# Optimization experiments

Hardware: AMD Instinct MI355X
Metric: run time of the kernel (lower is better)

The kernel has to match this reference:

```python
import jax, jax.numpy as jnp
import numpy as np

B, N, E, P, PH, H = 4, 512, 768, 64, 32, 8
D = E // H  # 96
FFN = 3072

def _ln(x, g, b, eps=1e-5):
    mu = jnp.mean(x, axis=-1, keepdims=True)
    var = jnp.mean((x - mu) ** 2, axis=-1, keepdims=True)
    return (x - mu) * jax.lax.rsqrt(var + eps) * g + b

def setup_inputs() -> dict:
    key = jax.random.key(0)
    ks = iter(jax.random.split(key, 80))
    def f(*s):
        return jax.random.normal(next(ks), s, jnp.float32) * 0.02
    ones = lambda *s: jnp.ones(s, jnp.float32)
    zeros = lambda *s: jnp.zeros(s, jnp.float32)
    return {
        'x': jax.random.normal(next(ks), (B, N, E), jnp.float32),
        'pair': jax.random.normal(next(ks), (B, N, N, P), jnp.float32) * 0.5,
        'attn_mask': zeros(B, 1, N, N),
        'op_mask': ones(B, N, 1),
        'op_norm': ones(1) / N,
        'nlist': jax.random.randint(next(ks), (B, N, 64), 0, N),
        'wq': f(E, E), 'wk': f(E, E), 'wv': f(E, E),
        'wg': f(E, E), 'bg': zeros(E),
        'wo': f(E, E), 'bo': zeros(E),
        'ln_pair_g': ones(P), 'ln_pair_b': zeros(P),
        'wb': f(H, P), 'bb': zeros(H),
        'ln_attn_g': ones(E), 'ln_attn_b': zeros(E),
        'ln_ffn_g': ones(E), 'ln_ffn_b': zeros(E),
        'w_ffn1': f(FFN, E), 'b_ffn1': zeros(FFN),
        'w_ffn2': f(E, FFN), 'b_ffn2': zeros(E),
        'ln_opm_g': ones(E), 'ln_opm_b': zeros(E),
        'w_opm_in': f(2 * PH, E), 'b_opm_in': zeros(2 * PH),
        'w_opm_out': f(P, PH * PH), 'b_opm_out': zeros(P),
        'ln_tm_g': ones(P), 'ln_tm_b': zeros(P),
        'w_tm_abp': f(2 * PH, P), 'b_tm_abp': zeros(2 * PH),
        'w_tm_abg': f(2 * PH, P), 'b_tm_abg': zeros(2 * PH),
        'w_tm_g': f(P, P), 'b_tm_g': zeros(P),
        'w_tm_z': f(P, PH), 'b_tm_z': zeros(P),
        'ln_tmo_g': ones(PH), 'ln_tmo_b': zeros(PH),
        'ln_pffn_g': ones(P), 'ln_pffn_b': zeros(P),
        'w_pffn1': f(P, P), 'b_pffn1': zeros(P),
        'w_pffn2': f(P, P), 'b_pffn2': zeros(P),
    }

def _forward(x, pair, attn_mask, op_mask, op_norm, wq, wk, wv, wg, bg, wo, bo,
             ln_pair_g, ln_pair_b, wb, bb, ln_attn_g, ln_attn_b,
             ln_ffn_g, ln_ffn_b, w_ffn1, b_ffn1, w_ffn2, b_ffn2,
             ln_opm_g, ln_opm_b, w_opm_in, b_opm_in, w_opm_out, b_opm_out,
             ln_tm_g, ln_tm_b, w_tm_abp, b_tm_abp, w_tm_abg, b_tm_abg,
             w_tm_g, b_tm_g, w_tm_z, b_tm_z, ln_tmo_g, ln_tmo_b,
             ln_pffn_g, ln_pffn_b, w_pffn1, b_pffn1, w_pffn2, b_pffn2):
    Bx, Nx, _ = x.shape
    # --- gated pair-bias self-attention (pre-LN, eval mode: dropout = identity) ---
    h = _ln(x, ln_attn_g, ln_attn_b)
    pn = _ln(pair, ln_pair_g, ln_pair_b)               # AtomAttention pair LayerNorm
    bias = jnp.einsum('bijp,hp->bhij', pn, wb) + bb[None, :, None, None]
    q = (h @ wq.T).reshape(Bx, Nx, H, D).transpose(0, 2, 1, 3) * (D ** -0.5)
    k = (h @ wk.T).reshape(Bx, Nx, H, D).transpose(0, 2, 1, 3)
    v = (h @ wv.T).reshape(Bx, Nx, H, D).transpose(0, 2, 1, 3)
    attn = jax.nn.softmax(jnp.einsum('bhid,bhjd->bhij', q, k) + attn_mask + bias, axis=-1)
    o = jnp.einsum('bhij,bhjd->bhid', attn, v).transpose(0, 2, 1, 3).reshape(Bx, Nx, E)
    o = jax.nn.sigmoid(h @ wg.T + bg) * o              # sigmoid output gate
    x = x + (o @ wo.T + bo)
    # --- atom transition MLP ---
    h = _ln(x, ln_ffn_g, ln_ffn_b)
    x = x + (jax.nn.gelu(h @ w_ffn1.T + b_ffn1, approximate=False) @ w_ffn2.T + b_ffn2)
    # --- OuterProduct pair update (fused: avoids [B,N,N,PH*PH] intermediate) ---
    h = _ln(x, ln_opm_g, ln_opm_b)
    ab = (h @ w_opm_in.T + b_opm_in) * op_mask
    a_o, b_o = jnp.split(ab, 2, axis=-1)               # each [B,N,PH]
    z = jnp.einsum('bid,bje,pde->bijp', a_o, b_o, w_opm_out.reshape(P, PH, PH)) + b_opm_out
    pair = pair + z * op_norm
    # --- triangle multiplication ---
    zp = _ln(pair, ln_tm_g, ln_tm_b)
    gpr = zp @ w_tm_g.T + b_tm_g                       # gate (no sigmoid, matches source)
    ab = (zp @ w_tm_abp.T + b_tm_abp) * jax.nn.sigmoid(zp @ w_tm_abg.T + b_tm_abg)
    a_t, b_t = jnp.split(ab, 2, axis=-1)               # each [B,N,N,PH]
    t = jnp.einsum('bijh,bkjh->bhik', a_t, b_t) + jnp.einsum('bjih,bjkh->bhik', a_t, b_t)
    t = _ln(t.transpose(0, 2, 3, 1), ln_tmo_g, ln_tmo_b) @ w_tm_z.T + b_tm_z
    pair = pair + gpr * t
    # --- pair transition MLP ---
    zp = _ln(pair, ln_pffn_g, ln_pffn_b)
    pair = pair + (jax.nn.gelu(zp @ w_pffn1.T + b_pffn1, approximate=False) @ w_pffn2.T + b_pffn2)
    return x, pair

def reference(x, pair, attn_mask, op_mask, op_norm, nlist, wq, wk, wv, wg, bg, wo, bo,
              ln_pair_g, ln_pair_b, wb, bb, ln_attn_g, ln_attn_b,
              ln_ffn_g, ln_ffn_b, w_ffn1, b_ffn1, w_ffn2, b_ffn2,
              ln_opm_g, ln_opm_b, w_opm_in, b_opm_in, w_opm_out, b_opm_out,
              ln_tm_g, ln_tm_b, w_tm_abp, b_tm_abp, w_tm_abg, b_tm_abg,
              w_tm_g, b_tm_g, w_tm_z, b_tm_z, ln_tmo_g, ln_tmo_b,
              ln_pffn_g, ln_pffn_b, w_pffn1, b_pffn1, w_pffn2, b_pffn2):
    del nlist  # accepted by the torch module but unused in the math
    return _forward(x, pair, attn_mask, op_mask, op_norm, wq, wk, wv, wg, bg, wo, bo,
                    ln_pair_g, ln_pair_b, wb, bb, ln_attn_g, ln_attn_b,
                    ln_ffn_g, ln_ffn_b, w_ffn1, b_ffn1, w_ffn2, b_ffn2,
                    ln_opm_g, ln_opm_b, w_opm_in, b_opm_in, w_opm_out, b_opm_out,
                    ln_tm_g, ln_tm_b, w_tm_abp, b_tm_abp, w_tm_abg, b_tm_abg,
                    w_tm_g, b_tm_g, w_tm_z, b_tm_z, ln_tmo_g, ln_tmo_b,
                    ln_pffn_g, ln_pffn_b, w_pffn1, b_pffn1, w_pffn2, b_pffn2)
```

## Files before the change

### kernel.cpp

```cpp
#include <hip/hip_runtime.h>
#include <hip/hip_bf16.h>
#include <math.h>

#define Nn 512
#define Ee 768
#define Pp 64
#define PHh 32
#define Hh 8
#define Dd 96
#define NNe 262144
#define LNEPS 1e-5f

typedef __attribute__((ext_vector_type(8))) short bf8;
typedef __attribute__((ext_vector_type(4))) short bf4;
typedef __attribute__((ext_vector_type(4))) float f32x4;
#define MFMA(a,b,c) __builtin_amdgcn_mfma_f32_16x16x32_bf16(a,b,c,0,0,0)

__device__ __forceinline__ short f2bf(float f) {
  unsigned u = __builtin_bit_cast(unsigned, f);
  unsigned r = (u + 0x7fffu + ((u >> 16) & 1u)) >> 16;
  return (short)r;
}
__device__ __forceinline__ float bf2f(short s) {
  unsigned u = ((unsigned)(unsigned short)s) << 16;
  return __builtin_bit_cast(float, u);
}

__device__ __forceinline__ float wave_red_sum(float v) {
#pragma unroll
  for (int off = 32; off > 0; off >>= 1) v += __shfl_xor(v, off);
  return v;
}
__device__ __forceinline__ float gelu_exact(float v) {
  return 0.5f * v * (1.f + erff(v * 0.70710678118654752f));
}
__device__ __forceinline__ float sigmoidf_(float v) {
  return 1.f / (1.f + expf(-v));
}

__global__ __launch_bounds__(256) void castw_kernel(
    const float* __restrict__ wq, const float* __restrict__ wk,
    const float* __restrict__ wv, const float* __restrict__ wg,
    const float* __restrict__ wo, const float* __restrict__ f1,
    const float* __restrict__ f2, const float* __restrict__ wop,
    short* __restrict__ dst, float qs) {
  long i = (long)blockIdx.x * 256 + threadIdx.x;
  float v;
  if (i < 589824) v = wq[i] * qs;
  else if (i < 1179648) v = wk[i - 589824];
  else if (i < 1769472) v = wv[i - 1179648];
  else if (i < 2359296) v = wg[i - 1769472];
  else if (i < 2949120) v = wo[i - 2359296];
  else if (i < 5308416) v = f1[i - 2949120];
  else if (i < 7667712) v = f2[i - 5308416];
  else if (i < 7716864) v = wop[i - 7667712];
  else return;
  dst[i] = f2bf(v);
}

__global__ __launch_bounds__(256) void castw2_kernel(
    const float* __restrict__ wb, const float* __restrict__ abp,
    const float* __restrict__ abg, const float* __restrict__ wtg,
    const float* __restrict__ wtz, const float* __restrict__ p1,
    const float* __restrict__ p2, short* __restrict__ dst) {
  int i = blockIdx.x * 256 + threadIdx.x;
  float v;
  if (i < 512) v = wb[i];
  else if (i < 4608) v = abp[i - 512];
  else if (i < 8704) v = abg[i - 4608];
  else if (i < 12800) v = wtg[i - 8704];
  else if (i < 14848) v = wtz[i - 12800];
  else if (i < 18944) v = p1[i - 14848];
  else if (i < 23040) v = p2[i - 18944];
  else return;
  dst[i] = f2bf(v);
}

__global__ __launch_bounds__(256) void ln_bf_kernel(const float* __restrict__ in,
                                                    short* __restrict__ out,
                                                    const float* __restrict__ gam,
                                                    const float* __restrict__ bet, int C) {
  int row = blockIdx.x;
  const float* xr = in + (long)row * C;
  short* yr = out + (long)row * C;
  float s = 0.f, ss = 0.f;
  for (int c = threadIdx.x; c < C; c += 256) { float v = xr[c]; s += v; ss += v * v; }
  s = wave_red_sum(s); ss = wave_red_sum(ss);
  __shared__ float sm[4][2];
  int wv = threadIdx.x >> 6, lane = threadIdx.x & 63;
  if (lane == 0) { sm[wv][0] = s; sm[wv][1] = ss; }
  __syncthreads();
  float ts = sm[0][0] + sm[1][0] + sm[2][0] + sm[3][0];
  float tss = sm[0][1] + sm[1][1] + sm[2][1] + sm[3][1];
  float mu = ts / C;
  float var = tss / C - mu * mu;
  float rs = rsqrtf(var + LNEPS);
  for (int c = threadIdx.x; c < C; c += 256) {
    float v = xr[c];
    yr[c] = f2bf((v - mu) * rs * gam[c] + bet[c]);
  }
}

__global__ __launch_bounds__(256) void gemm_bf(
    const short* __restrict__ A, int lda, long asB, long asH,
    const short* __restrict__ Bm, int ldb, long bsB, long bsH,
    float* __restrict__ outF, int ldf, long fsB, long fsH,
    short* __restrict__ outB, int ldob,
    const float* __restrict__ resid, int ldr, long rsB, long rsH,
    const float* __restrict__ bias,
    int M, int N, int K, int act, int vtrans, int Hdim) {
  int bz = blockIdx.z, bb = bz / Hdim, hh = bz % Hdim;
  A += bb * asB + hh * asH;
  Bm += bb * bsB + hh * bsH;
  if (outF) outF += bb * fsB + hh * fsH;
  if (outB) outB += bb * fsB + hh * fsH;
  if (resid) resid += bb * rsB + hh * rsH;
  __shared__ __align__(16) short As[64 * 72];
  __shared__ __align__(16) short Bs[64 * 72];
  int m0 = blockIdx.y * 64, n0 = blockIdx.x * 64;
  int tid = threadIdx.x;
  int wv = tid >> 6, lane = tid & 63;
  int wr = wv >> 1, wc = wv & 1;
  int lhi = lane >> 4, llo = lane & 15;
  int r4 = tid >> 2, c8 = (tid & 3) * 8;
  f32x4 acc[2][2] = {};
  for (int k0 = 0; k0 < K; k0 += 64) {
// ... 122 lines not shown
      }
    }
  }
}

__global__ __launch_bounds__(256) void gemm_ffn1(
    const short* __restrict__ A, const short* __restrict__ W,
    short* __restrict__ outB, const float* __restrict__ bias) {
  __shared__ __align__(16) short As[128 * 40];
  __shared__ __align__(16) short Bs[128 * 40];
  int m0 = blockIdx.y * 128, n0 = blockIdx.x * 128;
  int tid = threadIdx.x;
  int wv = tid >> 6, lane = tid & 63;
  int wr = wv >> 1, wc = wv & 1;
  int lhi = lane >> 4, llo = lane & 15;
  int r4 = tid >> 2, c8 = (tid & 3) * 8;
  f32x4 acc[4][4] = {};
  for (int k0 = 0; k0 < 768; k0 += 32) {
    *(bf8*)&As[r4 * 40 + c8] = *(const bf8*)(A + (long)(m0 + r4) * 768 + k0 + c8);
    *(bf8*)&As[(r4 + 64) * 40 + c8] =
        *(const bf8*)(A + (long)(m0 + r4 + 64) * 768 + k0 + c8);
    *(bf8*)&Bs[r4 * 40 + c8] = *(const bf8*)(W + (long)(n0 + r4) * 768 + k0 + c8);
    *(bf8*)&Bs[(r4 + 64) * 40 + c8] =
        *(const bf8*)(W + (long)(n0 + r4 + 64) * 768 + k0 + c8);
    __syncthreads();
    bf8 af[4], bfm[4];
#pragma unroll
    for (int mi = 0; mi < 4; ++mi)
      af[mi] = *(const bf8*)&As[(wr * 64 + mi * 16 + llo) * 40 + lhi * 8];
#pragma unroll
    for (int ni = 0; ni < 4; ++ni)
      bfm[ni] = *(const bf8*)&Bs[(wc * 64 + ni * 16 + llo) * 40 + lhi * 8];
#pragma unroll
    for (int mi = 0; mi < 4; ++mi)
#pragma unroll
      for (int ni = 0; ni < 4; ++ni)
        acc[mi][ni] = MFMA(af[mi], bfm[ni], acc[mi][ni]);
    __syncthreads();
  }
#pragma unroll
  for (int mi = 0; mi < 4; ++mi) {
    int gmb = m0 + wr * 64 + mi * 16 + lhi * 4;
#pragma unroll
    for (int ni = 0; ni < 4; ++ni) {
      int gn = n0 + wc * 64 + ni * 16 + llo;
      float bv = bias[gn];
#pragma unroll
      for (int r = 0; r < 4; ++r)
        outB[(long)(gmb + r) * 3072 + gn] = f2bf(gelu_exact(acc[mi][ni][r] + bv));
    }
  }
}

__global__ __launch_bounds__(256) void attn_fused(
    const short* __restrict__ q_bf, const short* __restrict__ k_bf,
    const short* __restrict__ bias_bf, const float* __restrict__ mask,
    short* __restrict__ out_bf) {
  int it = blockIdx.x, h = blockIdx.y, b = blockIdx.z;
  int tid = threadIdx.x;
  int wv = tid >> 6, lane = tid & 63;
  int lhi = lane >> 4, llo = lane & 15;
  int i0 = it * 16;
  long qoff = ((long)(b * 512 + i0)) * 768 + h * 96;
  bf8 qf[3];
#pragma unroll
  for (int ks = 0; ks < 3; ++ks)
    qf[ks] = *(const bf8*)(q_bf + qoff + (long)llo * 768 + ks * 32 + lhi * 8);
  long koff = ((long)b * 512) * 768 + h * 96;
  long bioff = (long)(b * 8 + h) * NNe + (long)i0 * 512;
  long moff = (long)b * NNe + (long)i0 * 512;
  float sv[8][4];
  int jb0 = wv * 128;
#pragma unroll
  for (int jf = 0; jf < 8; ++jf) {
    int jb = jb0 + jf * 16;
    f32x4 acc = {0.f, 0.f, 0.f, 0.f};
#pragma unroll
    for (int ks = 0; ks < 3; ++ks) {
      bf8 kf = *(const bf8*)(k_bf + koff + (long)(jb + llo) * 768 + ks * 32 + lhi * 8);
      acc = MFMA(qf[ks], kf, acc);
    }
#pragma unroll
    for (int r = 0; r < 4; ++r) {
      int irow = lhi * 4 + r;
      int j = jb + llo;
      float bia = bf2f(bias_bf[bioff + (long)irow * 512 + j]);
      float mk = mask[moff + (long)irow * 512 + j];
      sv[jf][r] = acc[r] + bia + mk;
    }
  }
  __shared__ float redA[4][20];
  __shared__ float redB[4][20];
  float rmax[4];
#pragma unroll
  for (int r = 0; r < 4; ++r) {
    float m = sv[0][r];
#pragma unroll
    for (int jf = 1; jf < 8; ++jf) m = fmaxf(m, sv[jf][r]);
#pragma unroll
    for (int off = 1; off < 16; off <<= 1) m = fmaxf(m, __shfl_xor(m, off, 16));
    if (llo == 0) redA[wv][lhi * 4 + r] = m;
  }
  __syncthreads();
#pragma unroll
  for (int r = 0; r < 4; ++r) {
    int row = lhi * 4 + r;
    rmax[r] = fmaxf(fmaxf(redA[0][row], redA[1][row]),
                    fmaxf(redA[2][row], redA[3][row]));
  }
  float rsum[4] = {0.f, 0.f, 0.f, 0.f};
#pragma unroll
  for (int jf = 0; jf < 8; ++jf)
#pragma unroll
    for (int r = 0; r < 4; ++r) {
      float e = __expf(sv[jf][r] - rmax[r]);
      sv[jf][r] = e;
      rsum[r] += e;
    }
#pragma unroll
  for (int r = 0; r < 4; ++r) {
#pragma unroll
    for (int off = 1; off < 16; off <<= 1) rsum[r] += __shfl_xor(rsum[r], off, 16);
    if (llo == 0) redB[wv][lhi * 4 + r] = rsum[r];
  }
  __syncthreads();
#pragma unroll
  for (int r = 0; r < 4; ++r) {
    int row = lhi * 4 + r;
    float s = redB[0][row] + redB[1][row] + redB[2][row] + redB[3][row];
    float inv = 1.f / s;
#pragma unroll
    for (int jf = 0; jf < 8; ++jf) {
      int j = jb0 + jf * 16 + llo;
      out_bf[bioff + (long)row * 512 + j] = f2bf(sv[jf][r] * inv);
    }
  }
}

__global__ __launch_bounds__(256) void opmask_kernel(float* __restrict__ ab,
                                                     const float* __restrict__ mask,
                                                     short* __restrict__ bo_bf) {
  int idx = blockIdx.x * 256 + threadIdx.x;
  if (idx < 131072) {
    float v = ab[idx] * mask[idx >> 6];
    ab[idx] = v;
    int ch = idx & 63;
    if (ch >= 32) bo_bf[(idx >> 6) * 32 + ch - 32] = f2bf(v);
  }
}

__global__ __launch_bounds__(256) void opm_T_kernel(const float* __restrict__ ab,
                                                    const float* __restrict__ w,
                                                    short* __restrict__ T) {
  int p = blockIdx.y;
  int row = blockIdx.x * 8 + threadIdx.y;
  int e = threadIdx.x;
  const float* a = ab + (long)row * 64;
  const float* wp = w + p * 1024 + e;
  float acc = 0.f;
#pragma unroll
  for (int d = 0; d < 32; ++d) acc += a[d] * wp[d * 32];
  T[((long)row * 64 + p) * 32 + e] = f2bf(acc);
}

__global__ __launch_bounds__(256) void pair_bias_mfma(
    const float* __restrict__ pair, const float* __restrict__ gam,
    const float* __restrict__ bet, const short* __restrict__ wb_a,
    const float* __restrict__ bbv, short* __restrict__ bias) {
  __shared__ __align__(16) short Zb[64 * 72];
  __shared__ __align__(16) short Wb[16 * 72];
  __shared__ float sp[4][2][72];
  int tid = threadIdx.x;
  long e0 = (long)blockIdx.x * 64;
  int b = (int)(e0 >> 18);
  long ein = e0 & (NNe - 1);
  const float* base = pair + e0 * 64;
  for (int l = tid; l < 1024; l += 256) {
    int h = l >> 6, c = l & 63;
    Wb[h * 72 + c] = (h < 8) ? wb_a[h * 64 + c] : (short)0;
  }
  int e = tid & 63, q = tid >> 6;
  f32x4 v4[4];
  float s = 0.f, ss = 0.f;
#pragma unroll
  for (int k = 0; k < 4; ++k) {
    v4[k] = *(const f32x4*)(base + (long)e * 64 + q * 16 + k * 4);
#pragma unroll
    for (int u = 0; u < 4; ++u) { float v = v4[k][u]; s += v; ss += v * v; }
  }
  sp[q][0][e] = s; sp[q][1][e] = ss;
  __syncthreads();
  float ts = sp[0][0][e] + sp[1][0][e] + sp[2][0][e] + sp[3][0][e];
  float tss = sp[0][1][e] + sp[1][1][e] + sp[2][1][e] + sp[3][1][e];
  float mu = ts * 0.015625f, var = tss * 0.015625f - mu * mu;
  float rs = rsqrtf(var + LNEPS);
#pragma unroll
  for (int k = 0; k < 4; ++k) {
    bf4 pk;
#pragma unroll
    for (int u = 0; u < 4; ++u) {
      int c = q * 16 + k * 4 + u;
      pk[u] = f2bf((v4[k][u] - mu) * rs * gam[c] + bet[c]);
    }
    *(bf4*)&Zb[e * 72 + q * 16 + k * 4] = pk;
  }
  __syncthreads();
  int wv = tid >> 6, lane = tid & 63;
  int lhi = lane >> 4, llo = lane & 15;
  int n0 = wv * 16;
  f32x4 acc = {0.f, 0.f, 0.f, 0.f};
#pragma unroll
  for (int ks = 0; ks < 2; ++ks) {
    bf8 a = *(const bf8*)&Wb[llo * 72 + ks * 32 + lhi * 8];
    bf8 bz = *(const bf8*)&Zb[(n0 + llo) * 72 + ks * 32 + lhi * 8];
    acc = MFMA(a, bz, acc);
  }
  int elem = n0 + llo;
#pragma unroll
  for (int r = 0; r < 4; ++r) {
    int h = lhi * 4 + r;
    if (h < 8) bias[(long)(b * 8 + h) * NNe + ein + elem] = f2bf(acc[r] + bbv[h]);
  }
}

__global__ __launch_bounds__(256) void opm_ab_fused(
    const float* __restrict__ pair_in, const short* __restrict__ Tb,
    const short* __restrict__ bo_bf, const float* __restrict__ b_out,
    const float* __restrict__ op_norm, const float* __restrict__ gam,
    const float* __restrict__ bet, const short* __restrict__ wp_a,
    const float* __restrict__ b_abp, const short* __restrict__ wg_a,
    const float* __restrict__ b_abg,
    short* __restrict__ aN, short* __restrict__ bN) {
  int jt = blockIdx.x;
  int i = blockIdx.y;
  int tid = threadIdx.x;
  __shared__ __align__(16) short Tsb[64 * 40];
  __shared__ __align__(16) short Bob[64 * 40];
  __shared__ __align__(16) short Zb[64 * 72];
  __shared__ __align__(16) short Wp[64 * 72];
  __shared__ __align__(16) short Wg[64 * 72];
  __shared__ float spS[64][9];
  __shared__ float spQ[64][9];
  int wv = tid >> 6, lane = tid & 63;
  int wr = wv >> 1, wc = wv & 1;
  int lhi = lane >> 4, llo = lane & 15;
  int chb = wr * 32 + lhi * 4;
  {
    int p = tid >> 2, e8 = (tid & 3) * 8;
    *(bf8*)&Tsb[p * 40 + e8] = *(const bf8*)(Tb + (long)i * 2048 + p * 32 + e8);
    *(bf8*)&Bob[p * 40 + e8] = *(const bf8*)(bo_bf + (long)(jt * 64 + p) * 32 + e8);
  }
  for (int l = tid; l < 512; l += 256) {
    int r = l >> 3, c8 = (l & 7) * 8;
    *(bf8*)&Wp[r * 72 + c8] = *(const bf8*)(wp_a + r * 64 + c8);
    *(bf8*)&Wg[r * 72 + c8] = *(const bf8*)(wg_a + r * 64 + c8);
  }
  long ebase = (long)i * 512 + jt * 64;
  const float* pbase = pair_in + ebase * 64;
  f32x4 x[2][2];
#pragma unroll
  for (int mi = 0; mi < 2; ++mi)
#pragma unroll
    for (int ni = 0; ni < 2; ++ni)
      x[mi][ni] = *(const f32x4*)(pbase + (long)(wc * 32 + ni * 16 + llo) * 64 +
                                  chb + mi * 16);
  __syncthreads();
  f32x4 acc[2][2] = {};
  {
    bf8 a0 = *(const bf8*)&Tsb[(wr * 32 + llo) * 40 + lhi * 8];
    bf8 a1 = *(const bf8*)&Tsb[(wr * 32 + 16 + llo) * 40 + lhi * 8];
    bf8 b0 = *(const bf8*)&Bob[(wc * 32 + llo) * 40 + lhi * 8];
    bf8 b1 = *(const bf8*)&Bob[(wc * 32 + 16 + llo) * 40 + lhi * 8];
    acc[0][0] = MFMA(a0, b0, acc[0][0]);
    acc[0][1] = MFMA(a0, b1, acc[0][1]);
    acc[1][0] = MFMA(a1, b0, acc[1][0]);
    acc[1][1] = MFMA(a1, b1, acc[1][1]);
  }
  float nrm = op_norm[0];
#pragma unroll
  for (int mi = 0; mi < 2; ++mi) {
    f32x4 bo4 = *(const f32x4*)(b_out + chb + mi * 16);
#pragma unroll
    for (int ni = 0; ni < 2; ++ni)
#pragma unroll
      for (int r = 0; r < 4; ++r)
        x[mi][ni][r] += (acc[mi][ni][r] + bo4[r]) * nrm;
  }
#pragma unroll
  for (int ni = 0; ni < 2; ++ni) {
    float s = 0.f, ss = 0.f;
#pragma unroll
    for (int mi = 0; mi < 2; ++mi)
#pragma unroll
      for (int r = 0; r < 4; ++r) { float v = x[mi][ni][r]; s += v; ss += v * v; }
    int e = wc * 32 + ni * 16 + llo;
    spS[e][wr * 4 + lhi] = s;
    spQ[e][wr * 4 + lhi] = ss;
  }
  __syncthreads();
  float mu1[2], rs1[2];
#pragma unroll
  for (int ni = 0; ni < 2; ++ni) {
    int e = wc * 32 + ni * 16 + llo;
    float s = 0.f, q2 = 0.f;
#pragma unroll
    for (int k = 0; k < 8; ++k) { s += spS[e][k]; q2 += spQ[e][k]; }
    float mu = s * 0.015625f, var = q2 * 0.015625f - mu * mu;
    mu1[ni] = mu; rs1[ni] = rsqrtf(var + LNEPS);
  }
#pragma unroll
  for (int mi = 0; mi < 2; ++mi) {
    f32x4 gv = *(const f32x4*)(gam + chb + mi * 16);
    f32x4 bv = *(const f32x4*)(bet + chb + mi * 16);
#pragma unroll
    for (int ni = 0; ni < 2; ++ni) {
      int e = wc * 32 + ni * 16 + llo;
      bf4 pk;
#pragma unroll
      for (int r = 0; r < 4; ++r)
        pk[r] = f2bf((x[mi][ni][r] - mu1[ni]) * rs1[ni] * gv[r] + bv[r]);
      *(bf4*)&Zb[e * 72 + chb + mi * 16] = pk;
    }
  }
  __syncthreads();
  f32x4 ap[2][2] = {};
  f32x4 ag[2][2] = {};
#pragma unroll
  for (int ks = 0; ks < 2; ++ks) {
    bf8 z0 = *(const bf8*)&Zb[(wr * 32 + llo) * 72 + ks * 32 + lhi * 8];
    bf8 z1 = *(const bf8*)&Zb[(wr * 32 + 16 + llo) * 72 + ks * 32 + lhi * 8];
    bf8 p0 = *(const bf8*)&Wp[(wc * 32 + llo) * 72 + ks * 32 + lhi * 8];
    bf8 p1 = *(const bf8*)&Wp[(wc * 32 + 16 + llo) * 72 + ks * 32 + lhi * 8];
    bf8 g0 = *(const bf8*)&Wg[(wc * 32 + llo) * 72 + ks * 32 + lhi * 8];
    bf8 g1 = *(const bf8*)&Wg[(wc * 32 + 16 + llo) * 72 + ks * 32 + lhi * 8];
    ap[0][0] = MFMA(z0, p0, ap[0][0]);
    ap[0][1] = MFMA(z0, p1, ap[0][1]);
    ap[1][0] = MFMA(z1, p0, ap[1][0]);
    ap[1][1] = MFMA(z1, p1, ap[1][1]);
    ag[0][0] = MFMA(z0, g0, ag[0][0]);
    ag[0][1] = MFMA(z0, g1, ag[0][1]);
    ag[1][0] = MFMA(z1, g0, ag[1][0]);
    ag[1][1] = MFMA(z1, g1, ag[1][1]);
  }
#pragma unroll
  for (int mi = 0; mi < 2; ++mi) {
    int elemb = wr * 32 + mi * 16 + lhi * 4;
#pragma unroll
    for (int ni = 0; ni < 2; ++ni) {
      int ch = wc * 32 + ni * 16 + llo;
      float bp = b_abp[ch], bg = b_abg[ch];
      bf4 pack;
#pragma unroll
      for (int r = 0; r < 4; ++r)
        pack[r] = f2bf((ap[mi][ni][r] + bp) * sigmoidf_(ag[mi][ni][r] + bg));
      short* dst = (ch < 32) ? (aN + (long)ch * NNe) : (bN + (long)(ch - 32) * NNe);
      *(bf4*)(dst + ebase + elemb) = pack;
    }
  }
}

__global__ __launch_bounds__(512) void tm_tri_mfma(const short* __restrict__ aN,
                                                   const short* __restrict__ bN,
                                                   short* __restrict__ t_out) {
  int lin = blockIdx.z * 16 + blockIdx.y * 4 + blockIdx.x;
  int vid = (lin & 7) * 64 + (lin >> 3);
  int h = vid >> 4;
  int rem = vid & 15;
  int i0 = (rem >> 2) * 128, k0 = (rem & 3) * 128;
  const short* A = aN + (long)h * NNe;
  const short* B = bN + (long)h * NNe;
  __shared__ __align__(16) short A1[128 * 40];
  __shared__ __align__(16) short B1[128 * 40];
  __shared__ __align__(16) short A2[128 * 40];
  __shared__ __align__(16) short B2[128 * 40];
  int tid = threadIdx.x;
  int wv = tid >> 6, lane = tid & 63;
  int wr = wv >> 2, wc = wv & 3;
  int lhi = lane >> 4, llo = lane & 15;
  int r1 = tid >> 2, cp = (tid & 3) * 8;
  int s2 = tid >> 5, cg = (tid & 31) * 4;
  f32x4 acc[4][2] = {};
  for (int j0 = 0; j0 < 512; j0 += 32) {
    *(bf8*)&A1[r1 * 40 + cp] = *(const bf8*)(A + (long)(i0 + r1) * 512 + j0 + cp);
    *(bf8*)&B1[r1 * 40 + cp] = *(const bf8*)(B + (long)(k0 + r1) * 512 + j0 + cp);
    bf4 va0 = *(const bf4*)(A + (long)(j0 + 2 * s2) * 512 + i0 + cg);
    bf4 va1 = *(const bf4*)(A + (long)(j0 + 2 * s2 + 1) * 512 + i0 + cg);
    bf4 vb0 = *(const bf4*)(B + (long)(j0 + 2 * s2) * 512 + k0 + cg);
    bf4 vb1 = *(const bf4*)(B + (long)(j0 + 2 * s2 + 1) * 512 + k0 + cg);
#pragma unroll
    for (int q = 0; q < 4; ++q) {
      unsigned pa = (unsigned)(unsigned short)va0[q] |
                    ((unsigned)(unsigned short)va1[q] << 16);
      unsigned pb = (unsigned)(unsigned short)vb0[q] |
                    ((unsigned)(unsigned short)vb1[q] << 16);
      *(unsigned*)&A2[(cg + q) * 40 + 2 * s2] = pa;
      *(unsigned*)&B2[(cg + q) * 40 + 2 * s2] = pb;
    }
    __syncthreads();
    bf8 bfr[2], dfr[2];
#pragma unroll
    for (int ni = 0; ni < 2; ++ni) {
      bfr[ni] = *(const bf8*)&B1[(wc * 32 + ni * 16 + llo) * 40 + lhi * 8];
      dfr[ni] = *(const bf8*)&B2[(wc * 32 + ni * 16 + llo) * 40 + lhi * 8];
    }
#pragma unroll
    for (int mi = 0; mi < 4; ++mi) {
      bf8 a = *(const bf8*)&A1[(wr * 64 + mi * 16 + llo) * 40 + lhi * 8];
      acc[mi][0] = MFMA(a, bfr[0], acc[mi][0]);
      acc[mi][1] = MFMA(a, bfr[1], acc[mi][1]);
    }
#pragma unroll
    for (int mi = 0; mi < 4; ++mi) {
      bf8 c = *(const bf8*)&A2[(wr * 64 + mi * 16 + llo) * 40 + lhi * 8];
      acc[mi][0] = MFMA(c, dfr[0], acc[mi][0]);
      acc[mi][1] = MFMA(c, dfr[1], acc[mi][1]);
    }
    __syncthreads();
  }
  short* tp = t_out + (long)h * NNe;
#pragma unroll
  for (int mi = 0; mi < 4; ++mi)
#pragma unroll
    for (int ni = 0; ni < 2; ++ni) {
      int row = i0 + wr * 64 + mi * 16 + lhi * 4;
      int col = k0 + wc * 32 + ni * 16 + llo;
#pragma unroll
      for (int r = 0; r < 4; ++r) tp[(long)(row + r) * 512 + col] = f2bf(acc[mi][ni][r]);
    }
}

__global__ __launch_bounds__(256) void upd_pffn_fused(
    const float* __restrict__ pin, float* __restrict__ pout,
    const short* __restrict__ t_in,
    const short* __restrict__ Tb, const short* __restrict__ bo_bf,
    const float* __restrict__ b_out, const float* __restrict__ op_norm,
    const float* __restrict__ g_tm, const float* __restrict__ b_tm,
    const short* __restrict__ wg_a, const float* __restrict__ b_g,
    const short* __restrict__ wz_a, const float* __restrict__ b_z,
    const float* __restrict__ g_tmo, const float* __restrict__ b_tmo,
    const float* __restrict__ g_pf, const float* __restrict__ b_pf,
    const short* __restrict__ w1_a, const float* __restrict__ b1,
    const short* __restrict__ w2_a, const float* __restrict__ b2) {
  __shared__ __align__(16) short Zb[64 * 72];
  __shared__ __align__(16) short Tlb[64 * 40];
  __shared__ __align__(16) short Wbuf[64 * 72];
  __shared__ __align__(16) short Wzb[64 * 40];
  __shared__ __align__(16) short Tsb[64 * 40];
  __shared__ __align__(16) short Bob[64 * 40];
  __shared__ float spS[64][9];
  __shared__ float spQ[64][9];
  __shared__ float spB[4][2][72];
  int tid = threadIdx.x;
  long e0 = (long)blockIdx.x * 64;
  int i = (int)(e0 >> 9);
  int jt = (int)((e0 >> 6) & 7);
  int wv = tid >> 6, lane = tid & 63;
  int wr = wv >> 1, wc = wv & 1;
  int lhi = lane >> 4, llo = lane & 15;
  int chb = wr * 32 + lhi * 4;
  int r0 = tid >> 3, c0 = (tid & 7) * 8;
  int r1 = (tid + 256) >> 3, c1 = ((tid + 256) & 7) * 8;
  bf8 w1r0, w1r1, w2r0, w2r1;
  {
    *(bf8*)&Wbuf[r0 * 72 + c0] = *(const bf8*)(wg_a + r0 * 64 + c0);
    *(bf8*)&Wbuf[r1 * 72 + c1] = *(const bf8*)(wg_a + r1 * 64 + c1);
    w1r0 = *(const bf8*)(w1_a + r0 * 64 + c0);
    w1r1 = *(const bf8*)(w1_a + r1 * 64 + c1);
    w2r0 = *(const bf8*)(w2_a + r0 * 64 + c0);
    w2r1 = *(const bf8*)(w2_a + r1 * 64 + c1);
    int rz = tid >> 2, cz = (tid & 3) * 8;
    *(bf8*)&Wzb[rz * 40 + cz] = *(const bf8*)(wz_a + rz * 32 + cz);
    int p = tid >> 2, e8 = (tid & 3) * 8;
    *(bf8*)&Tsb[p * 40 + e8] = *(const bf8*)(Tb + (long)i * 2048 + p * 32 + e8);
    *(bf8*)&Bob[p * 40 + e8] = *(const bf8*)(bo_bf + (long)(jt * 64 + p) * 32 + e8);
  }
  f32x4 x[2][2];
#pragma unroll
  for (int mi = 0; mi < 2; ++mi)
#pragma unroll
    for (int ni = 0; ni < 2; ++ni)
      x[mi][ni] = *(const f32x4*)(pin + (e0 + wc * 32 + ni * 16 + llo) * 64 +
                                  chb + mi * 16);
  int te = tid & 63, tq = tid >> 6;
  float tt[8];
  {
    float sB = 0.f, ssB = 0.f;
#pragma unroll
    for (int k = 0; k < 8; ++k) {
      float v = bf2f(t_in[(long)(tq * 8 + k) * NNe + e0 + te]);
      tt[k] = v; sB += v; ssB += v * v;
    }
    spB[tq][0][te] = sB; spB[tq][1][te] = ssB;
  }
  __syncthreads();
  {
    float ts = spB[0][0][te] + spB[1][0][te] + spB[2][0][te] + spB[3][0][te];
    float tss = spB[0][1][te] + spB[1][1][te] + spB[2][1][te] + spB[3][1][te];
    float mu = ts * 0.03125f, var = tss * 0.03125f - mu * mu;
    float rs = rsqrtf(var + LNEPS);
    bf8 pk;
#pragma unroll
    for (int k = 0; k < 8; ++k) {
      int c = tq * 8 + k;
      pk[k] = f2bf((tt[k] - mu) * rs * g_tmo[c] + b_tmo[c]);
    }
    *(bf8*)&Tlb[te * 40 + tq * 8] = pk;
  }
  {
    f32x4 acc[2][2] = {};
    bf8 a0 = *(const bf8*)&Tsb[(wr * 32 + llo) * 40 + lhi * 8];
    bf8 a1 = *(const bf8*)&Tsb[(wr * 32 + 16 + llo) * 40 + lhi * 8];
    bf8 b0 = *(const bf8*)&Bob[(wc * 32 + llo) * 40 + lhi * 8];
    bf8 b1 = *(const bf8*)&Bob[(wc * 32 + 16 + llo) * 40 + lhi * 8];
    acc[0][0] = MFMA(a0, b0, acc[0][0]);
    acc[0][1] = MFMA(a0, b1, acc[0][1]);
    acc[1][0] = MFMA(a1, b0, acc[1][0]);
    acc[1][1] = MFMA(a1, b1, acc[1][1]);
    float nrm = op_norm[0];
#pragma unroll
    for (int mi = 0; mi < 2; ++mi) {
      f32x4 bo4 = *(const f32x4*)(b_out + chb + mi * 16);
#pragma unroll
      for (int ni = 0; ni < 2; ++ni)
#pragma unroll
        for (int r = 0; r < 4; ++r)
          x[mi][ni][r] += (acc[mi][ni][r] + bo4[r]) * nrm;
    }
  }
#pragma unroll
  for (int ni = 0; ni < 2; ++ni) {
    float s = 0.f, ss = 0.f;
#pragma unroll
    for (int mi = 0; mi < 2; ++mi)
#pragma unroll
      for (int r = 0; r < 4; ++r) { float v = x[mi][ni][r]; s += v; ss += v * v; }
    int e = wc * 32 + ni * 16 + llo;
    spS[e][wr * 4 + lhi] = s;
    spQ[e][wr * 4 + lhi] = ss;
  }
  __syncthreads();
  float mu1[2], rs1[2];
#pragma unroll
// ... 172 lines not shown
  const float* w_ffn2 = (const float*)d_in[23];
  const float* b_ffn2 = (const float*)d_in[24];
  const float* ln_opm_g = (const float*)d_in[25];
  const float* ln_opm_b = (const float*)d_in[26];
  const float* w_opm_in = (const float*)d_in[27];
  const float* b_opm_in = (const float*)d_in[28];
  const float* w_opm_out = (const float*)d_in[29];
  const float* b_opm_out = (const float*)d_in[30];
  const float* ln_tm_g = (const float*)d_in[31];
  const float* ln_tm_b = (const float*)d_in[32];
  const float* w_tm_abp = (const float*)d_in[33];
  const float* b_tm_abp = (const float*)d_in[34];
  const float* w_tm_abg = (const float*)d_in[35];
  const float* b_tm_abg = (const float*)d_in[36];
  const float* w_tm_g = (const float*)d_in[37];
  const float* b_tm_g = (const float*)d_in[38];
  const float* w_tm_z = (const float*)d_in[39];
  const float* b_tm_z = (const float*)d_in[40];
  const float* ln_tmo_g = (const float*)d_in[41];
  const float* ln_tmo_b = (const float*)d_in[42];
  const float* ln_pffn_g = (const float*)d_in[43];
  const float* ln_pffn_b = (const float*)d_in[44];
  const float* w_pffn1 = (const float*)d_in[45];
  const float* b_pffn1 = (const float*)d_in[46];
  const float* w_pffn2 = (const float*)d_in[47];
  const float* b_pffn2 = (const float*)d_in[48];

  float* ws = (float*)d_ws;
  short* wbf = (short*)ws;
  short* wq_bf = wbf + 0;
  short* wo_bf = wbf + 2359296;
  short* wf1_bf = wbf + 2949120;
  short* wf2_bf = wbf + 5308416;
  short* wop_bf = wbf + 7667712;
  short* wb_a = wbf + 7716864;
  short* wabp_a = wbf + 7717376;
  short* wabg_a = wbf + 7721472;
  short* wtg_a = wbf + 7725568;
  short* wtz_a = wbf + 7729664;
  short* wp1_a = wbf + 7731712;
  short* wp2_a = wbf + 7735808;

  short* h_bf = (short*)(ws + 3869952);
  short* q_bf = (short*)(ws + 4656384);
  short* k_bf = (short*)(ws + 5442816);
  short* vT_bf = (short*)(ws + 6229248);
  float* gb = ws + 7015680;
  short* gb_bf = (short*)(ws + 10161408);
  float* x1b = ws + 10947840;
  short* biasb_bf = (short*)(ws + 12520704);
  short* attn_bf = (short*)(ws + 16715008);
  short* mffn_bf = (short*)(ws + 20909312);
  float* abb = ws + 24055040;
  short* abb_bf = (short*)(ws + 24186112);
  short* Tb_bf = (short*)(ws + 24218880);
  short* aNb = (short*)(ws + 4656384);
  short* bNb = (short*)(ws + 8850688);
  short* t_bf = (short*)(ws + 13044992);

  float* xo = (float*)d_out;
  float* pair1 = xo + 1572864;

  const float qscale = 0.1020620726159658f;

  castw_kernel<<<30144, 256, 0, stream>>>(wq, wk, wv_, wg, wo, w_ffn1, w_ffn2, w_opm_in,
                                          wbf, qscale);
  castw2_kernel<<<90, 256, 0, stream>>>(wb, w_tm_abp, w_tm_abg, w_tm_g, w_tm_z,
                                        w_pffn1, w_pffn2, wb_a);
  ln_bf_kernel<<<2048, 256, 0, stream>>>(x, h_bf, ln_attn_g, ln_attn_b, 768);
  gemm_qkvg<<<dim3(24, 16, 1), 256, 0, stream>>>(h_bf, wq_bf, q_bf, k_bf, vT_bf, gb, bg);
  pair_bias_mfma<<<16384, 256, 0, stream>>>(pair, ln_pair_g, ln_pair_b, wb_a, bb, biasb_bf);
  attn_fused<<<dim3(32, 8, 4), 256, 0, stream>>>(q_bf, k_bf, biasb_bf, attn_mask, attn_bf);
  gemm_bf<<<dim3(2, 8, 32), 256, 0, stream>>>(attn_bf, 512, 2097152, 262144,
                                              vT_bf, 512, 393216, 49152,
                                              nullptr, 0, 393216, 96, gb_bf, 768,
                                              gb, 768, 393216, 96, nullptr,
                                              512, 96, 512, 2, 0, 8);
  gemm_bf<<<dim3(12, 32, 1), 256, 0, stream>>>(gb_bf, 768, 0, 0, wo_bf, 768, 0, 0,
                                               x1b, 768, 0, 0, nullptr, 0,
                                               x, 768, 0, 0, bo,
                                               2048, 768, 768, 0, 0, 1);
  ln_bf_kernel<<<2048, 256, 0, stream>>>(x1b, h_bf, ln_ffn_g, ln_ffn_b, 768);
  gemm_ffn1<<<dim3(24, 16, 1), 256, 0, stream>>>(h_bf, wf1_bf, mffn_bf, b_ffn1);
  gemm_bf<<<dim3(12, 32, 1), 256, 0, stream>>>(mffn_bf, 3072, 0, 0, wf2_bf, 3072, 0, 0,
                                               xo, 768, 0, 0, nullptr, 0,
                                               x1b, 768, 0, 0, b_ffn2,
                                               2048, 768, 3072, 0, 0, 1);
  ln_bf_kernel<<<2048, 256, 0, stream>>>(xo, h_bf, ln_opm_g, ln_opm_b, 768);
  gemm_bf<<<dim3(1, 32, 1), 256, 0, stream>>>(h_bf, 768, 0, 0, wop_bf, 768, 0, 0,
                                              abb, 64, 0, 0, nullptr, 0,
                                              nullptr, 0, 0, 0, b_opm_in,
                                              2048, 64, 768, 0, 0, 1);
  opmask_kernel<<<512, 256, 0, stream>>>(abb, op_mask, abb_bf);
  opm_T_kernel<<<dim3(256, 64, 1), dim3(32, 8, 1), 0, stream>>>(abb, w_opm_out, Tb_bf);
  for (int b = 0; b < 4; ++b) {
    const float* pin = pair + (long)b * NNe * 64;
    float* pbb = pair1 + (long)b * NNe * 64;
    opm_ab_fused<<<dim3(8, 512, 1), 256, 0, stream>>>(
        pin, Tb_bf + (long)b * 1048576, abb_bf + (long)b * 16384, b_opm_out, op_norm,
        ln_tm_g, ln_tm_b, wabp_a, b_tm_abp, wabg_a, b_tm_abg, aNb, bNb);
    tm_tri_mfma<<<dim3(4, 4, 32), 512, 0, stream>>>(aNb, bNb, t_bf);
    upd_pffn_fused<<<4096, 256, 0, stream>>>(
        pin, pbb, t_bf, Tb_bf + (long)b * 1048576, abb_bf + (long)b * 16384,
        b_opm_out, op_norm,
        ln_tm_g, ln_tm_b, wtg_a, b_tm_g, wtz_a, b_tm_z,
        ln_tmo_g, ln_tmo_b, ln_pffn_g, ln_pffn_b, wp1_a, b_pffn1, wp2_a, b_pffn2);
  }
}
```

Baseline: 907.0 us.

## Batch pair-track kernels across batch, cache bf16 pair copy, merge small kernels

Removes the per-batch loop so opm_ab_fused, tm_tri_mfma and upd_pffn_fused each launch once over all four batches, backed by larger workspace buffers. pair_bias_mfma now also writes a bf16 copy of pair, which later kernels read instead of the fp32 tensor, halving that traffic. The two weight-cast kernels are merged, opmask is folded into opm_T_kernel, and the two N=768 output GEMMs move to a new 128x128-tile kernel. Reading pair as bf16 in the residual path adds precision loss, and the extra bf16 write plus the larger workspace add memory cost.

```diff
diff --git a/kernel.cpp b/kernel.cpp
--- a/kernel.cpp
+++ b/kernel.cpp
@@ -43,6 +43,10 @@
     const float* __restrict__ wv, const float* __restrict__ wg,
     const float* __restrict__ wo, const float* __restrict__ f1,
     const float* __restrict__ f2, const float* __restrict__ wop,
+    const float* __restrict__ wb, const float* __restrict__ abp,
+    const float* __restrict__ abg, const float* __restrict__ wtg,
+    const float* __restrict__ wtz, const float* __restrict__ p1,
+    const float* __restrict__ p2,
     short* __restrict__ dst, float qs) {
   long i = (long)blockIdx.x * 256 + threadIdx.x;
   float v;
@@ -54,24 +58,13 @@
   else if (i < 5308416) v = f1[i - 2949120];
   else if (i < 7667712) v = f2[i - 5308416];
   else if (i < 7716864) v = wop[i - 7667712];
-  else return;
-  dst[i] = f2bf(v);
-}
-
-__global__ __launch_bounds__(256) void castw2_kernel(
-    const float* __restrict__ wb, const float* __restrict__ abp,
-    const float* __restrict__ abg, const float* __restrict__ wtg,
-    const float* __restrict__ wtz, const float* __restrict__ p1,
-    const float* __restrict__ p2, short* __restrict__ dst) {
-  int i = blockIdx.x * 256 + threadIdx.x;
-  float v;
-  if (i < 512) v = wb[i];
-  else if (i < 4608) v = abp[i - 512];
-  else if (i < 8704) v = abg[i - 4608];
-  else if (i < 12800) v = wtg[i - 8704];
-  else if (i < 14848) v = wtz[i - 12800];
-  else if (i < 18944) v = p1[i - 14848];
-  else if (i < 23040) v = p2[i - 18944];
+  else if (i < 7717376) v = wb[i - 7716864];
+  else if (i < 7721472) v = abp[i - 7717376];
+  else if (i < 7725568) v = abg[i - 7721472];
+  else if (i < 7729664) v = wtg[i - 7725568];
+  else if (i < 7731712) v = wtz[i - 7729664];
+  else if (i < 7735808) v = p1[i - 7731712];
+  else if (i < 7739904) v = p2[i - 7735808];
   else return;
   dst[i] = f2bf(v);
 }
@@ -300,6 +293,56 @@
   }
 }
 
+__global__ __launch_bounds__(256) void gemm128(
+    const short* __restrict__ A, const short* __restrict__ W, int K,
+    const float* __restrict__ resid, const float* __restrict__ bias,
+    float* __restrict__ outF) {
+  __shared__ __align__(16) short As[128 * 40];
+  __shared__ __align__(16) short Bs[128 * 40];
+  int m0 = blockIdx.y * 128, n0 = blockIdx.x * 128;
+  int tid = threadIdx.x;
+  int wv = tid >> 6, lane = tid & 63;
+  int wr = wv >> 1, wc = wv & 1;
+  int lhi = lane >> 4, llo = lane & 15;
+  int r4 = tid >> 2, c8 = (tid & 3) * 8;
+  f32x4 acc[4][4] = {};
+  for (int k0 = 0; k0 < K; k0 += 32) {
+    *(bf8*)&As[r4 * 40 + c8] = *(const bf8*)(A + (long)(m0 + r4) * K + k0 + c8);
+    *(bf8*)&As[(r4 + 64) * 40 + c8] =
+        *(const bf8*)(A + (long)(m0 + r4 + 64) * K + k0 + c8);
+    *(bf8*)&Bs[r4 * 40 + c8] = *(const bf8*)(W + (long)(n0 + r4) * K + k0 + c8);
+    *(bf8*)&Bs[(r4 + 64) * 40 + c8] =
+        *(const bf8*)(W + (long)(n0 + r4 + 64) * K + k0 + c8);
+    __syncthreads();
+    bf8 af[4], bfm[4];
+#pragma unroll
+    for (int mi = 0; mi < 4; ++mi)
+      af[mi] = *(const bf8*)&As[(wr * 64 + mi * 16 + llo) * 40 + lhi * 8];
+#pragma unroll
+    for (int ni = 0; ni < 4; ++ni)
+      bfm[ni] = *(const bf8*)&Bs[(wc * 64 + ni * 16 + llo) * 40 + lhi * 8];
+#pragma unroll
+    for (int mi = 0; mi < 4; ++mi)
+#pragma unroll
+      for (int ni = 0; ni < 4; ++ni)
+        acc[mi][ni] = MFMA(af[mi], bfm[ni], acc[mi][ni]);
+    __syncthreads();
+  }
+#pragma unroll
+  for (int mi = 0; mi < 4; ++mi) {
+    int gmb = m0 + wr * 64 + mi * 16 + lhi * 4;
+#pragma unroll
+    for (int ni = 0; ni < 4; ++ni) {
+      int gn = n0 + wc * 64 + ni * 16 + llo;
+      float bv = bias[gn];
+#pragma unroll
+      for (int r = 0; r < 4; ++r)
+        outF[(long)(gmb + r) * 768 + gn] =
+            acc[mi][ni][r] + bv + resid[(long)(gmb + r) * 768 + gn];
+    }
+  }
+}
+
 __global__ __launch_bounds__(256) void attn_fused(
     const short* __restrict__ q_bf, const short* __restrict__ k_bf,
     const short* __restrict__ bias_bf, const float* __restrict__ mask,
@@ -385,36 +428,29 @@
   }
 }
 
-__global__ __launch_bounds__(256) void opmask_kernel(float* __restrict__ ab,
-                                                     const float* __restrict__ mask,
-                                                     short* __restrict__ bo_bf) {
-  int idx = blockIdx.x * 256 + threadIdx.x;
-  if (idx < 131072) {
-    float v = ab[idx] * mask[idx >> 6];
-    ab[idx] = v;
-    int ch = idx & 63;
-    if (ch >= 32) bo_bf[(idx >> 6) * 32 + ch - 32] = f2bf(v);
-  }
-}
-
 __global__ __launch_bounds__(256) void opm_T_kernel(const float* __restrict__ ab,
+                                                    const float* __restrict__ mask,
                                                     const float* __restrict__ w,
-                                                    short* __restrict__ T) {
+                                                    short* __restrict__ T,
+                                                    short* __restrict__ bo_bf) {
   int p = blockIdx.y;
   int row = blockIdx.x * 8 + threadIdx.y;
   int e = threadIdx.x;
+  float mk = mask[row];
   const float* a = ab + (long)row * 64;
   const float* wp = w + p * 1024 + e;
   float acc = 0.f;
 #pragma unroll
   for (int d = 0; d < 32; ++d) acc += a[d] * wp[d * 32];
-  T[((long)row * 64 + p) * 32 + e] = f2bf(acc);
+  T[((long)row * 64 + p) * 32 + e] = f2bf(acc * mk);
+  if (blockIdx.y == 0) bo_bf[(long)row * 32 + e] = f2bf(a[32 + e] * mk);
 }
 
 __global__ __launch_bounds__(256) void pair_bias_mfma(
     const float* __restrict__ pair, const float* __restrict__ gam,
     const float* __restrict__ bet, const short* __restrict__ wb_a,
-    const float* __restrict__ bbv, short* __restrict__ bias) {
+    const float* __restrict__ bbv, short* __restrict__ bias,
+    short* __restrict__ pair_bf) {
   __shared__ __align__(16) short Zb[64 * 72];
   __shared__ __align__(16) short Wb[16 * 72];
   __shared__ float sp[4][2][72];
@@ -436,6 +472,13 @@
 #pragma unroll
     for (int u = 0; u < 4; ++u) { float v = v4[k][u]; s += v; ss += v * v; }
   }
+#pragma unroll
+  for (int k = 0; k < 4; ++k) {
+    bf4 pr;
+#pragma unroll
+    for (int u = 0; u < 4; ++u) pr[u] = f2bf(v4[k][u]);
+    *(bf4*)(pair_bf + (e0 + e) * 64 + q * 16 + k * 4) = pr;
+  }
   sp[q][0][e] = s; sp[q][1][e] = ss;
   __syncthreads();
   float ts = sp[0][0][e] + sp[1][0][e] + sp[2][0][e] + sp[3][0][e];
@@ -472,15 +515,16 @@
 }
 
 __global__ __launch_bounds__(256) void opm_ab_fused(
-    const float* __restrict__ pair_in, const short* __restrict__ Tb,
+    const short* __restrict__ pair_bf, const short* __restrict__ Tb,
     const short* __restrict__ bo_bf, const float* __restrict__ b_out,
     const float* __restrict__ op_norm, const float* __restrict__ gam,
     const float* __restrict__ bet, const short* __restrict__ wp_a,
     const float* __restrict__ b_abp, const short* __restrict__ wg_a,
     const float* __restrict__ b_abg,
-    short* __restrict__ aN, short* __restrict__ bN) {
+    short* __restrict__ aN4, short* __restrict__ bN4) {
   int jt = blockIdx.x;
   int i = blockIdx.y;
+  int bb = blockIdx.z;
   int tid = threadIdx.x;
   __shared__ __align__(16) short Tsb[64 * 40];
   __shared__ __align__(16) short Bob[64 * 40];
@@ -493,10 +537,12 @@
   int wr = wv >> 1, wc = wv & 1;
   int lhi = lane >> 4, llo = lane & 15;
   int chb = wr * 32 + lhi * 4;
+  long grow = (long)bb * 512 + i;
   {
     int p = tid >> 2, e8 = (tid & 3) * 8;
-    *(bf8*)&Tsb[p * 40 + e8] = *(const bf8*)(Tb + (long)i * 2048 + p * 32 + e8);
-    *(bf8*)&Bob[p * 40 + e8] = *(const bf8*)(bo_bf + (long)(jt * 64 + p) * 32 + e8);
+    *(bf8*)&Tsb[p * 40 + e8] = *(const bf8*)(Tb + grow * 2048 + p * 32 + e8);
+    *(bf8*)&Bob[p * 40 + e8] =
+        *(const bf8*)(bo_bf + ((long)bb * 512 + jt * 64 + p) * 32 + e8);
   }
   for (int l = tid; l < 512; l += 256) {
     int r = l >> 3, c8 = (l & 7) * 8;
@@ -504,14 +550,19 @@
     *(bf8*)&Wg[r * 72 + c8] = *(const bf8*)(wg_a + r * 64 + c8);
   }
   long ebase = (long)i * 512 + jt * 64;
-  const float* pbase = pair_in + ebase * 64;
+  const short* pbase = pair_bf + ((long)bb * NNe + ebase) * 64;
+  short* aN = aN4 + (long)bb * 8388608;
+  short* bN = bN4 + (long)bb * 8388608;
   f32x4 x[2][2];
 #pragma unroll
   for (int mi = 0; mi < 2; ++mi)
 #pragma unroll
-    for (int ni = 0; ni < 2; ++ni)
-      x[mi][ni] = *(const f32x4*)(pbase + (long)(wc * 32 + ni * 16 + llo) * 64 +
-                                  chb + mi * 16);
+    for (int ni = 0; ni < 2; ++ni) {
+      bf4 pv = *(const bf4*)(pbase + (long)(wc * 32 + ni * 16 + llo) * 64 +
+                             chb + mi * 16);
+#pragma unroll
+      for (int r = 0; r < 4; ++r) x[mi][ni][r] = bf2f(pv[r]);
+    }
   __syncthreads();
   f32x4 acc[2][2] = {};
   {
@@ -607,16 +658,17 @@
   }
 }
 
-__global__ __launch_bounds__(512) void tm_tri_mfma(const short* __restrict__ aN,
-                                                   const short* __restrict__ bN,
-                                                   short* __restrict__ t_out) {
+__global__ __launch_bounds__(512) void tm_tri_mfma(const short* __restrict__ aN4,
+                                                   const short* __restrict__ bN4,
+                                                   short* __restrict__ t4) {
   int lin = blockIdx.z * 16 + blockIdx.y * 4 + blockIdx.x;
-  int vid = (lin & 7) * 64 + (lin >> 3);
-  int h = vid >> 4;
+  int vid = (lin & 7) * 256 + (lin >> 3);
+  int hh = vid >> 4;
+  int b = hh >> 5, h = hh & 31;
   int rem = vid & 15;
   int i0 = (rem >> 2) * 128, k0 = (rem & 3) * 128;
-  const short* A = aN + (long)h * NNe;
-  const short* B = bN + (long)h * NNe;
+  const short* A = aN4 + (long)b * 8388608 + (long)h * NNe;
+  const short* B = bN4 + (long)b * 8388608 + (long)h * NNe;
   __shared__ __align__(16) short A1[128 * 40];
   __shared__ __align__(16) short B1[128 * 40];
   __shared__ __align__(16) short A2[128 * 40];
@@ -665,7 +717,7 @@
     }
     __syncthreads();
   }
-  short* tp = t_out + (long)h * NNe;
+  short* tp = t4 + (long)b * 8388608 + (long)h * NNe;
 #pragma unroll
   for (int mi = 0; mi < 4; ++mi)
 #pragma unroll
@@ -678,8 +730,8 @@
 }
 
 __global__ __launch_bounds__(256) void upd_pffn_fused(
-    const float* __restrict__ pin, float* __restrict__ pout,
-    const short* __restrict__ t_in,
+    const short* __restrict__ pair_bf, float* __restrict__ pout,
+    const short* __restrict__ t4,
     const short* __restrict__ Tb, const short* __restrict__ bo_bf,
     const float* __restrict__ b_out, const float* __restrict__ op_norm,
     const float* __restrict__ g_tm, const float* __restrict__ b_tm,
@@ -700,7 +752,9 @@
   __shared__ float spB[4][2][72];
   int tid = threadIdx.x;
   long e0 = (long)blockIdx.x * 64;
-  int i = (int)(e0 >> 9);
+  int bbt = (int)(e0 >> 18);
+  long el = e0 & (NNe - 1);
+  long growT = e0 >> 9;
   int jt = (int)((e0 >> 6) & 7);
   int wv = tid >> 6, lane = tid & 63;
   int wr = wv >> 1, wc = wv & 1;
@@ -719,23 +773,28 @@
     int rz = tid >> 2, cz = (tid & 3) * 8;
     *(bf8*)&Wzb[rz * 40 + cz] = *(const bf8*)(wz_a + rz * 32 + cz);
     int p = tid >> 2, e8 = (tid & 3) * 8;
-    *(bf8*)&Tsb[p * 40 + e8] = *(const bf8*)(Tb + (long)i * 2048 + p * 32 + e8);
-    *(bf8*)&Bob[p * 40 + e8] = *(const bf8*)(bo_bf + (long)(jt * 64 + p) * 32 + e8);
+    *(bf8*)&Tsb[p * 40 + e8] = *(const bf8*)(Tb + growT * 2048 + p * 32 + e8);
+    *(bf8*)&Bob[p * 40 + e8] =
+        *(const bf8*)(bo_bf + ((long)bbt * 512 + jt * 64 + p) * 32 + e8);
   }
   f32x4 x[2][2];
 #pragma unroll
   for (int mi = 0; mi < 2; ++mi)
 #pragma unroll
-    for (int ni = 0; ni < 2; ++ni)
-      x[mi][ni] = *(const f32x4*)(pin + (e0 + wc * 32 + ni * 16 + llo) * 64 +
-                                  chb + mi * 16);
+    for (int ni = 0; ni < 2; ++ni) {
+      bf4 pv = *(const bf4*)(pair_bf + (e0 + wc * 32 + ni * 16 + llo) * 64 +
+                             chb + mi * 16);
+#pragma unroll
+      for (int r = 0; r < 4; ++r) x[mi][ni][r] = bf2f(pv[r]);
+    }
+  const short* t_in = t4 + (long)bbt * 8388608;
   int te = tid & 63, tq = tid >> 6;
   float tt[8];
   {
     float sB = 0.f, ssB = 0.f;
 #pragma unroll
     for (int k = 0; k < 8; ++k) {
-      float v = bf2f(t_in[(long)(tq * 8 + k) * NNe + e0 + te]);
+      float v = bf2f(t_in[(long)(tq * 8 + k) * NNe + el + te]);
       tt[k] = v; sB += v; ssB += v * v;
     }
     spB[tq][0][te] = sB; spB[tq][1][te] = ssB;
@@ -1014,58 +1073,48 @@
   short* attn_bf = (short*)(ws + 16715008);
   short* mffn_bf = (short*)(ws + 20909312);
   float* abb = ws + 24055040;
-  short* abb_bf = (short*)(ws + 24186112);
+  short* bo_bf = (short*)(ws + 24186112);
   short* Tb_bf = (short*)(ws + 24218880);
-  short* aNb = (short*)(ws + 4656384);
-  short* bNb = (short*)(ws + 8850688);
-  short* t_bf = (short*)(ws + 13044992);
+  short* pair_bfp = (short*)(ws + 26316032);
+  short* aN4 = (short*)(ws + 59870464);
+  short* bN4 = (short*)(ws + 76647680);
+  short* t4 = (short*)(ws + 93424896);
 
   float* xo = (float*)d_out;
   float* pair1 = xo + 1572864;
 
   const float qscale = 0.1020620726159658f;
 
-  castw_kernel<<<30144, 256, 0, stream>>>(wq, wk, wv_, wg, wo, w_ffn1, w_ffn2, w_opm_in,
-                                          wbf, qscale);
-  castw2_kernel<<<90, 256, 0, stream>>>(wb, w_tm_abp, w_tm_abg, w_tm_g, w_tm_z,
-                                        w_pffn1, w_pffn2, wb_a);
+  castw_kernel<<<30234, 256, 0, stream>>>(wq, wk, wv_, wg, wo, w_ffn1, w_ffn2, w_opm_in,
+                                          wb, w_tm_abp, w_tm_abg, w_tm_g, w_tm_z,
+                                          w_pffn1, w_pffn2, wbf, qscale);
   ln_bf_kernel<<<2048, 256, 0, stream>>>(x, h_bf, ln_attn_g, ln_attn_b, 768);
   gemm_qkvg<<<dim3(24, 16, 1), 256, 0, stream>>>(h_bf, wq_bf, q_bf, k_bf, vT_bf, gb, bg);
-  pair_bias_mfma<<<16384, 256, 0, stream>>>(pair, ln_pair_g, ln_pair_b, wb_a, bb, biasb_bf);
+  pair_bias_mfma<<<16384, 256, 0, stream>>>(pair, ln_pair_g, ln_pair_b, wb_a, bb,
+                                            biasb_bf, pair_bfp);
   attn_fused<<<dim3(32, 8, 4), 256, 0, stream>>>(q_bf, k_bf, biasb_bf, attn_mask, attn_bf);
   gemm_bf<<<dim3(2, 8, 32), 256, 0, stream>>>(attn_bf, 512, 2097152, 262144,
                                               vT_bf, 512, 393216, 49152,
                                               nullptr, 0, 393216, 96, gb_bf, 768,
                                               gb, 768, 393216, 96, nullptr,
                                               512, 96, 512, 2, 0, 8);
-  gemm_bf<<<dim3(12, 32, 1), 256, 0, stream>>>(gb_bf, 768, 0, 0, wo_bf, 768, 0, 0,
-                                               x1b, 768, 0, 0, nullptr, 0,
-                                               x, 768, 0, 0, bo,
-                                               2048, 768, 768, 0, 0, 1);
+  gemm128<<<dim3(6, 16, 1), 256, 0, stream>>>(gb_bf, wo_bf, 768, x, bo, x1b);
   ln_bf_kernel<<<2048, 256, 0, stream>>>(x1b, h_bf, ln_ffn_g, ln_ffn_b, 768);
   gemm_ffn1<<<dim3(24, 16, 1), 256, 0, stream>>>(h_bf, wf1_bf, mffn_bf, b_ffn1);
-  gemm_bf<<<dim3(12, 32, 1), 256, 0, stream>>>(mffn_bf, 3072, 0, 0, wf2_bf, 3072, 0, 0,
-                                               xo, 768, 0, 0, nullptr, 0,
-                                               x1b, 768, 0, 0, b_ffn2,
-                                               2048, 768, 3072, 0, 0, 1);
+  gemm128<<<dim3(6, 16, 1), 256, 0, stream>>>(mffn_bf, wf2_bf, 3072, x1b, b_ffn2, xo);
   ln_bf_kernel<<<2048, 256, 0, stream>>>(xo, h_bf, ln_opm_g, ln_opm_b, 768);
   gemm_bf<<<dim3(1, 32, 1), 256, 0, stream>>>(h_bf, 768, 0, 0, wop_bf, 768, 0, 0,
                                               abb, 64, 0, 0, nullptr, 0,
                                               nullptr, 0, 0, 0, b_opm_in,
                                               2048, 64, 768, 0, 0, 1);
-  opmask_kernel<<<512, 256, 0, stream>>>(abb, op_mask, abb_bf);
-  opm_T_kernel<<<dim3(256, 64, 1), dim3(32, 8, 1), 0, stream>>>(abb, w_opm_out, Tb_bf);
-  for (int b = 0; b < 4; ++b) {
-    const float* pin = pair + (long)b * NNe * 64;
-    float* pbb = pair1 + (long)b * NNe * 64;
-    opm_ab_fused<<<dim3(8, 512, 1), 256, 0, stream>>>(
-        pin, Tb_bf + (long)b * 1048576, abb_bf + (long)b * 16384, b_opm_out, op_norm,
-        ln_tm_g, ln_tm_b, wabp_a, b_tm_abp, wabg_a, b_tm_abg, aNb, bNb);
-    tm_tri_mfma<<<dim3(4, 4, 32), 512, 0, stream>>>(aNb, bNb, t_bf);
-    upd_pffn_fused<<<4096, 256, 0, stream>>>(
-        pin, pbb, t_bf, Tb_bf + (long)b * 1048576, abb_bf + (long)b * 16384,
-        b_opm_out, op_norm,
-        ln_tm_g, ln_tm_b, wtg_a, b_tm_g, wtz_a, b_tm_z,
-        ln_tmo_g, ln_tmo_b, ln_pffn_g, ln_pffn_b, wp1_a, b_pffn1, wp2_a, b_pffn2);
-  }
-}
+  opm_T_kernel<<<dim3(256, 64, 1), dim3(32, 8, 1), 0, stream>>>(abb, op_mask, w_opm_out,
+                                                                Tb_bf, bo_bf);
+  opm_ab_fused<<<dim3(8, 512, 4), 256, 0, stream>>>(
+      pair_bfp, Tb_bf, bo_bf, b_opm_out, op_norm,
+      ln_tm_g, ln_tm_b, wabp_a, b_tm_abp, wabg_a, b_tm_abg, aN4, bN4);
+  tm_tri_mfma<<<dim3(4, 4, 128), 512, 0, stream>>>(aN4, bN4, t4);
+  upd_pffn_fused<<<16384, 256, 0, stream>>>(
+      pair_bfp, pair1, t4, Tb_bf, bo_bf, b_opm_out, op_norm,
+      ln_tm_g, ln_tm_b, wtg_a, b_tm_g, wtz_a, b_tm_z,
+      ln_tmo_g, ln_tmo_b, ln_pffn_g, ln_pffn_b, wp1_a, b_pffn1, wp2_a, b_pffn2);
+}
```

Measured after the change: 940.5 us. +3.7%, slower.
